# Kernel optimization log

Hardware: AMD Instinct MI355X
Metric: run time of the kernel (lower is better)

Reference implementation:

```python
import jax, jax.numpy as jnp
import numpy as np

M, N, D, P = 16, 4096, 128, 8192
H = N // D


def setup_inputs() -> dict:
    key = jax.random.key(0)
    ks = jax.random.split(key, 6)
    s = 1.0 / np.sqrt(N)
    return {
        "X": jax.random.normal(ks[0], (M, N), dtype=jnp.float32),
        "W_q": jax.random.normal(ks[1], (N, N), dtype=jnp.float32) * s,
        "W_k": jax.random.normal(ks[2], (N, N), dtype=jnp.float32) * s,
        "W_v": jax.random.normal(ks[3], (N, N), dtype=jnp.float32) * s,
        "cache_K": jax.random.normal(ks[4], (H, P, D), dtype=jnp.float32),
        "cache_V": jax.random.normal(ks[5], (H, P, D), dtype=jnp.float32),
    }


def reference(X, W_q, W_k, W_v, cache_K, cache_V):
    m = X.shape[0]
    h, p, d = cache_K.shape
    # QKV projections: [M, N] @ [N, N] -> [M, H, D] -> [H, M, D]
    q = (X @ W_q).reshape(m, h, d).transpose(1, 0, 2)
    k = (X @ W_k).reshape(m, h, d).transpose(1, 0, 2)
    v = (X @ W_v).reshape(m, h, d).transpose(1, 0, 2)
    # KV-cache concat along the sequence axis -> [H, P+M, D]
    k_all = jnp.concatenate([cache_K, k], axis=1)
    v_all = jnp.concatenate([cache_V, v], axis=1)
    # attention (note: original applies NO 1/sqrt(D) scaling)
    scores = jnp.einsum('hmd,hpd->hmp', q, k_all)  # [H, M, P+M]
    weights = jax.nn.softmax(scores, axis=-1)
    out = jnp.einsum('hmp,hpd->hmd', weights, v_all)  # [H, M, D]
    return out.transpose(1, 0, 2).reshape(m, h * d)
```

## Files before the change

### kernel.cpp

```cpp
#include <hip/hip_runtime.h>

#define HN 32
#define MM 16
#define DD 128
#define NN 4096
#define PP 8192
#define TP 64
#define NCH 32
#define CROWS 256

__global__ __launch_bounds__(256) void qkv_kernel(
    const float* __restrict__ X, const float* __restrict__ Wq,
    const float* __restrict__ Wk, const float* __restrict__ Wv,
    float* __restrict__ qkv)
{
    const int bx  = blockIdx.x;
    const int mat = bx >> 8;
    const int r   = bx & 255;
    const int ct  = r >> 5;
    const int rc  = r & 31;
    const int col0 = ct << 9;
    const int i0   = rc << 7;
    const float* W = (mat == 0) ? Wq : (mat == 1) ? Wk : Wv;
    const int t = threadIdx.x;

    const int c0 = col0 + t, c1 = col0 + 256 + t;
    float a0[MM], a1[MM];
#pragma unroll
    for (int m = 0; m < MM; ++m) { a0[m] = 0.f; a1[m] = 0.f; }

    for (int i8 = 0; i8 < 128; i8 += 8) {
        const float* Wr = W + (size_t)(i0 + i8) * NN;
        float w0[8], w1[8];
#pragma unroll
        for (int rr = 0; rr < 8; ++rr) {
            w0[rr] = Wr[(size_t)rr*NN + c0];
            w1[rr] = Wr[(size_t)rr*NN + c1];
        }
        const float* Xr = X + i0 + i8;
#pragma unroll
        for (int m = 0; m < MM; ++m) {
            float4 xa = *reinterpret_cast<const float4*>(Xr + (size_t)m*NN);
            float4 xb = *reinterpret_cast<const float4*>(Xr + (size_t)m*NN + 4);
            a0[m] += xa.x*w0[0] + xa.y*w0[1] + xa.z*w0[2] + xa.w*w0[3]
                   + xb.x*w0[4] + xb.y*w0[5] + xb.z*w0[6] + xb.w*w0[7];
            a1[m] += xa.x*w1[0] + xa.y*w1[1] + xa.z*w1[2] + xa.w*w1[3]
                   + xb.x*w1[4] + xb.y*w1[5] + xb.z*w1[6] + xb.w*w1[7];
        }
    }
    float* base = qkv + (size_t)mat * HN*MM*DD;
    const int h0 = c0 >> 7, d0 = c0 & 127;
    const int h1 = c1 >> 7, d1 = c1 & 127;
#pragma unroll
    for (int m = 0; m < MM; ++m) {
        atomicAdd(&base[(h0*MM + m)*DD + d0], a0[m]);
        atomicAdd(&base[(h1*MM + m)*DD + d1], a1[m]);
    }
}

__global__ __launch_bounds__(256, 2) void attn_partial6(
    const float* __restrict__ cacheK, const float* __restrict__ cacheV,
    const float* __restrict__ qkv, float* __restrict__ pmu,
    float* __restrict__ ps, float* __restrict__ pacc)
{
    __shared__ float Ks[TP][DD + 4];
    __shared__ float Wl[TP][20];

    const int chunk = blockIdx.x;
    const int h     = blockIdx.y;
    const int t     = threadIdx.x;
    const int lane  = t & 63;
    const int wv    = __builtin_amdgcn_readfirstlane((int)(threadIdx.x >> 6));
    const int srow  = t >> 5;
    const int sg    = t & 31;
    const int psi   = lane >> 4;
    const int g     = lane & 15;

    const float* k_ws = qkv + HN*MM*DD;
    const float* v_ws = qkv + 2*HN*MM*DD;
    const int start = chunk * CROWS;
    const float* Kbase = cacheK + ((size_t)h*PP + start)*DD;
    const float* Vbase = cacheV + ((size_t)h*PP + start)*DD;
    const float* qb    = qkv + ((size_t)h*MM + 4*wv)*DD;

    const int ntile = 4 + (chunk == NCH - 1 ? 1 : 0);

    float mu0 = -3.0e38f, mu1 = -3.0e38f, mu2 = -3.0e38f, mu3 = -3.0e38f;
    float ss0 = 0.f, ss1 = 0.f, ss2 = 0.f, ss3 = 0.f;
    float acc[4][8];
#pragma unroll
    for (int q = 0; q < 4; ++q)
#pragma unroll
        for (int k = 0; k < 8; ++k) acc[q][k] = 0.f;

    for (int tt = 0; tt < ntile; ++tt) {
        const bool tail  = (tt == 4);
        const int  valid = tail ? MM : TP;

        const float* srcK = tail ? k_ws + (size_t)h*MM*DD
                                 : Kbase + (size_t)tt*TP*DD;
#pragma unroll
        for (int rr = 0; rr < 8; ++rr) {
            const int row  = srow + 8*rr;
            const int srcr = tail ? min(row, MM - 1) : row;
            float4 kk = *reinterpret_cast<const float4*>(srcK + (size_t)srcr*DD + sg*4);
            *reinterpret_cast<float4*>(&Ks[row][sg*4]) = kk;
        }
        __syncthreads();

        float s0 = 0.f, s1 = 0.f, s2 = 0.f, s3 = 0.f;
#pragma unroll 8
        for (int dq = 0; dq < 32; ++dq) {
            float4 k  = *reinterpret_cast<const float4*>(&Ks[lane][dq*4]);
            const float* qp = qb + dq*4;
            float4 q0 = *reinterpret_cast<const float4*>(qp);
            float4 q1 = *reinterpret_cast<const float4*>(qp + DD);
            float4 q2 = *reinterpret_cast<const float4*>(qp + 2*DD);
            float4 q3 = *reinterpret_cast<const float4*>(qp + 3*DD);
            s0 += k.x*q0.x + k.y*q0.y + k.z*q0.z + k.w*q0.w;
            s1 += k.x*q1.x + k.y*q1.y + k.z*q1.z + k.w*q1.w;
            s2 += k.x*q2.x + k.y*q2.y + k.z*q2.z + k.w*q2.w;
            s3 += k.x*q3.x + k.y*q3.y + k.z*q3.z + k.w*q3.w;
        }
        if (lane >= valid) { s0 = s1 = s2 = s3 = -3.0e38f; }

        float m0 = s0, m1 = s1, m2 = s2, m3 = s3;
#pragma unroll
        for (int off = 1; off < 64; off <<= 1) {
            m0 = fmaxf(m0, __shfl_xor(m0, off));
            m1 = fmaxf(m1, __shfl_xor(m1, off));
            m2 = fmaxf(m2, __shfl_xor(m2, off));
            m3 = fmaxf(m3, __shfl_xor(m3, off));
        }
        const float n0 = fmaxf(mu0, m0), n1 = fmaxf(mu1, m1);
        const float n2 = fmaxf(mu2, m2), n3 = fmaxf(mu3, m3);
        const float r0 = __expf(mu0 - n0), r1 = __expf(mu1 - n1);
        const float r2 = __expf(mu2 - n2), r3 = __expf(mu3 - n3);
        const float w0 = __expf(s0 - n0);
        const float w1 = __expf(s1 - n1);
        const float w2 = __expf(s2 - n2);
        const float w3 = __expf(s3 - n3);
        float t0s = w0, t1s = w1, t2s = w2, t3s = w3;
#pragma unroll
        for (int off = 1; off < 64; off <<= 1) {
            t0s += __shfl_xor(t0s, off);
            t1s += __shfl_xor(t1s, off);
            t2s += __shfl_xor(t2s, off);
            t3s += __shfl_xor(t3s, off);
        }
        ss0 = ss0*r0 + t0s; ss1 = ss1*r1 + t1s;
        ss2 = ss2*r2 + t2s; ss3 = ss3*r3 + t3s;
        mu0 = n0; mu1 = n1; mu2 = n2; mu3 = n3;
        *reinterpret_cast<float4*>(&Wl[lane][4*wv]) = make_float4(w0, w1, w2, w3);

        __syncthreads();

#pragma unroll
        for (int k = 0; k < 8; ++k) {
            acc[0][k] *= r0; acc[1][k] *= r1; acc[2][k] *= r2; acc[3][k] *= r3;
        }
        const float* srcV = tail ? v_ws + (size_t)h*MM*DD
                                 : Vbase + (size_t)tt*TP*DD;
#pragma unroll 4
        for (int i = 0; i < 16; ++i) {
            const int p    = psi + 4*i;
            const int srcr = tail ? min(p, MM - 1) : p;
            const float* vp = srcV + (size_t)srcr*DD + g*8;
            float4 wq = *reinterpret_cast<const float4*>(&Wl[p][4*wv]);
            float4 v0 = *reinterpret_cast<const float4*>(vp);
            float4 v1 = *reinterpret_cast<const float4*>(vp + 4);
            acc[0][0] += wq.x*v0.x; acc[0][1] += wq.x*v0.y; acc[0][2] += wq.x*v0.z; acc[0][3] += wq.x*v0.w;
            acc[0][4] += wq.x*v1.x; acc[0][5] += wq.x*v1.y; acc[0][6] += wq.x*v1.z; acc[0][7] += wq.x*v1.w;
            acc[1][0] += wq.y*v0.x; acc[1][1] += wq.y*v0.y; acc[1][2] += wq.y*v0.z; acc[1][3] += wq.y*v0.w;
            acc[1][4] += wq.y*v1.x; acc[1][5] += wq.y*v1.y; acc[1][6] += wq.y*v1.z; acc[1][7] += wq.y*v1.w;
            acc[2][0] += wq.z*v0.x; acc[2][1] += wq.z*v0.y; acc[2][2] += wq.z*v0.z; acc[2][3] += wq.z*v0.w;
            acc[2][4] += wq.z*v1.x; acc[2][5] += wq.z*v1.y; acc[2][6] += wq.z*v1.z; acc[2][7] += wq.z*v1.w;
            acc[3][0] += wq.w*v0.x; acc[3][1] += wq.w*v0.y; acc[3][2] += wq.w*v0.z; acc[3][3] += wq.w*v0.w;
            acc[3][4] += wq.w*v1.x; acc[3][5] += wq.w*v1.y; acc[3][6] += wq.w*v1.z; acc[3][7] += wq.w*v1.w;
        }
    }

#pragma unroll
    for (int q = 0; q < 4; ++q)
#pragma unroll
        for (int k = 0; k < 8; ++k) {
            float v = acc[q][k];
            v += __shfl_xor(v, 16);
            v += __shfl_xor(v, 32);
            acc[q][k] = v;
        }
    if (lane < 16) {
        float* pa = pacc + ((size_t)(h*NCH + chunk)*MM + 4*wv)*DD;
#pragma unroll
        for (int q = 0; q < 4; ++q) {
            *reinterpret_cast<float4*>(pa + q*DD + g*8) =
                make_float4(acc[q][0], acc[q][1], acc[q][2], acc[q][3]);
            *reinterpret_cast<float4*>(pa + q*DD + g*8 + 4) =
                make_float4(acc[q][4], acc[q][5], acc[q][6], acc[q][7]);
        }
    }
    if (lane == 0) {
        const int o = (h*NCH + chunk)*MM + 4*wv;
        pmu[o + 0] = mu0; pmu[o + 1] = mu1; pmu[o + 2] = mu2; pmu[o + 3] = mu3;
        ps [o + 0] = ss0; ps [o + 1] = ss1; ps [o + 2] = ss2; ps [o + 3] = ss3;
    }
}

__global__ __launch_bounds__(128) void combine_kernel(
    const float* __restrict__ pmu, const float* __restrict__ ps,
    const float* __restrict__ pacc, float* __restrict__ out)
{
    const int b = blockIdx.x;
    const int h = b >> 4, m = b & 15;
    const int d = threadIdx.x;
    float gm = -3.0e38f;
#pragma unroll 8
    for (int c = 0; c < NCH; ++c)
        gm = fmaxf(gm, pmu[(h*NCH + c)*MM + m]);
    float stot = 0.f, a = 0.f;
#pragma unroll 8
    for (int c = 0; c < NCH; ++c) {
        const float f = __expf(pmu[(h*NCH + c)*MM + m] - gm);
        stot += ps[(h*NCH + c)*MM + m] * f;
        a += pacc[((size_t)(h*NCH + c)*MM + m)*DD + d] * f;
    }
    out[m*NN + h*DD + d] = a / stot;
}

extern "C" void kernel_launch(void* const* d_in, const int* in_sizes, int n_in,
                              void* d_out, int out_size, void* d_ws, size_t ws_size,
                              hipStream_t stream) {
    const float* X  = (const float*)d_in[0];
    const float* Wq = (const float*)d_in[1];
    const float* Wk = (const float*)d_in[2];
    const float* Wv = (const float*)d_in[3];
    const float* cK = (const float*)d_in[4];
    const float* cV = (const float*)d_in[5];
    float* out = (float*)d_out;

    float* ws     = (float*)d_ws;
    float* qkv    = ws;
    float* pmu_p  = ws + 3*HN*MM*DD;
    float* ps_p   = pmu_p + HN*NCH*MM;
    float* pacc_p = ps_p + HN*NCH*MM;

    hipMemsetAsync(qkv, 0, (size_t)3*HN*MM*DD*sizeof(float), stream);
    qkv_kernel<<<768, 256, 0, stream>>>(X, Wq, Wk, Wv, qkv);
    attn_partial6<<<dim3(NCH, HN), 256, 0, stream>>>(cK, cV, qkv, pmu_p, ps_p, pacc_p);
    combine_kernel<<<HN*MM, 128, 0, stream>>>(pmu_p, ps_p, pacc_p, out);
}
```

Baseline: 177.6 us.

## Replace QKV atomics with split-K partials plus reduce, halve attention chunks, prefetch K

The QKV projection no longer uses memset plus atomicAdd. Each split-K block writes its partial sums to workspace, and a separate reduce kernel sums them into qkv. The attention kernel now uses 64 chunks of 128 rows instead of 32 of 256, which doubles the grid for more parallelism. It also prefetches the next K tile into registers while the current one is being used. This adds an extra kernel launch and extra workspace traffic for the partials, and raises register pressure in the attention kernel.

```diff
diff --git a/kernel.cpp b/kernel.cpp
--- a/kernel.cpp
+++ b/kernel.cpp
@@ -6,21 +6,22 @@
 #define NN 4096
 #define PP 8192
 #define TP 64
-#define NCH 32
-#define CROWS 256
+#define NCH 64
+#define CROWS 128
 
 __global__ __launch_bounds__(256) void qkv_kernel(
     const float* __restrict__ X, const float* __restrict__ Wq,
     const float* __restrict__ Wk, const float* __restrict__ Wv,
-    float* __restrict__ qkv)
-{
-    const int bx  = blockIdx.x;
-    const int mat = bx >> 8;
-    const int r   = bx & 255;
-    const int ct  = r >> 5;
-    const int rc  = r & 31;
+    float* __restrict__ part, int RC)
+{
+    const int bx   = blockIdx.x;
+    const int mat  = bx / (8 * RC);
+    const int rem  = bx - mat * 8 * RC;
+    const int ct   = rem / RC;
+    const int rcid = rem - ct * RC;
+    const int ROWS = NN / RC;
     const int col0 = ct << 9;
-    const int i0   = rc << 7;
+    const int i0   = rcid * ROWS;
     const float* W = (mat == 0) ? Wq : (mat == 1) ? Wk : Wv;
     const int t = threadIdx.x;
 
@@ -29,36 +30,56 @@
 #pragma unroll
     for (int m = 0; m < MM; ++m) { a0[m] = 0.f; a1[m] = 0.f; }
 
-    for (int i8 = 0; i8 < 128; i8 += 8) {
-        const float* Wr = W + (size_t)(i0 + i8) * NN;
-        float w0[8], w1[8];
-#pragma unroll
-        for (int rr = 0; rr < 8; ++rr) {
+    for (int ib = 0; ib < ROWS; ib += 16) {
+        const float* Wr = W + (size_t)(i0 + ib) * NN;
+        float w0[16], w1[16];
+#pragma unroll
+        for (int rr = 0; rr < 16; ++rr) {
             w0[rr] = Wr[(size_t)rr*NN + c0];
             w1[rr] = Wr[(size_t)rr*NN + c1];
         }
-        const float* Xr = X + i0 + i8;
+        const float* Xr = X + i0 + ib;
 #pragma unroll
         for (int m = 0; m < MM; ++m) {
             float4 xa = *reinterpret_cast<const float4*>(Xr + (size_t)m*NN);
             float4 xb = *reinterpret_cast<const float4*>(Xr + (size_t)m*NN + 4);
+            float4 xc = *reinterpret_cast<const float4*>(Xr + (size_t)m*NN + 8);
+            float4 xd = *reinterpret_cast<const float4*>(Xr + (size_t)m*NN + 12);
             a0[m] += xa.x*w0[0] + xa.y*w0[1] + xa.z*w0[2] + xa.w*w0[3]
-                   + xb.x*w0[4] + xb.y*w0[5] + xb.z*w0[6] + xb.w*w0[7];
+                   + xb.x*w0[4] + xb.y*w0[5] + xb.z*w0[6] + xb.w*w0[7]
+                   + xc.x*w0[8] + xc.y*w0[9] + xc.z*w0[10] + xc.w*w0[11]
+                   + xd.x*w0[12] + xd.y*w0[13] + xd.z*w0[14] + xd.w*w0[15];
             a1[m] += xa.x*w1[0] + xa.y*w1[1] + xa.z*w1[2] + xa.w*w1[3]
-                   + xb.x*w1[4] + xb.y*w1[5] + xb.z*w1[6] + xb.w*w1[7];
-        }
-    }
-    float* base = qkv + (size_t)mat * HN*MM*DD;
-    const int h0 = c0 >> 7, d0 = c0 & 127;
-    const int h1 = c1 >> 7, d1 = c1 & 127;
+                   + xb.x*w1[4] + xb.y*w1[5] + xb.z*w1[6] + xb.w*w1[7]
+                   + xc.x*w1[8] + xc.y*w1[9] + xc.z*w1[10] + xc.w*w1[11]
+                   + xd.x*w1[12] + xd.y*w1[13] + xd.z*w1[14] + xd.w*w1[15];
+        }
+    }
+    float* pb = part + ((size_t)(rcid*3 + mat)*MM)*NN;
 #pragma unroll
     for (int m = 0; m < MM; ++m) {
-        atomicAdd(&base[(h0*MM + m)*DD + d0], a0[m]);
-        atomicAdd(&base[(h1*MM + m)*DD + d1], a1[m]);
-    }
-}
-
-__global__ __launch_bounds__(256, 2) void attn_partial6(
+        pb[(size_t)m*NN + c0] = a0[m];
+        pb[(size_t)m*NN + c1] = a1[m];
+    }
+}
+
+__global__ __launch_bounds__(256) void qkv_reduce(
+    const float* __restrict__ part, float* __restrict__ qkv, int RC)
+{
+    const int o   = blockIdx.x * 256 + threadIdx.x;
+    const int mat = o >> 16;
+    const int r   = o & 65535;
+    const int h   = r >> 11;
+    const int m   = (r >> 7) & 15;
+    const int d   = r & 127;
+    const int col = h * DD + d;
+    const float* p = part + ((size_t)mat*MM + m)*NN + col;
+    float s = 0.f;
+    for (int rc = 0; rc < RC; ++rc) s += p[(size_t)rc * (3*MM*NN)];
+    qkv[o] = s;
+}
+
+__global__ __launch_bounds__(256, 2) void attn_partial7(
     const float* __restrict__ cacheK, const float* __restrict__ cacheV,
     const float* __restrict__ qkv, float* __restrict__ pmu,
     float* __restrict__ ps, float* __restrict__ pacc)
@@ -83,7 +104,7 @@
     const float* Vbase = cacheV + ((size_t)h*PP + start)*DD;
     const float* qb    = qkv + ((size_t)h*MM + 4*wv)*DD;
 
-    const int ntile = 4 + (chunk == NCH - 1 ? 1 : 0);
+    const int ntile = 2 + (chunk == NCH - 1 ? 1 : 0);
 
     float mu0 = -3.0e38f, mu1 = -3.0e38f, mu2 = -3.0e38f, mu3 = -3.0e38f;
     float ss0 = 0.f, ss1 = 0.f, ss2 = 0.f, ss3 = 0.f;
@@ -93,19 +114,33 @@
 #pragma unroll
         for (int k = 0; k < 8; ++k) acc[q][k] = 0.f;
 
+    float4 stK[8];
+    auto issueK = [&](int tt2) {
+        if (tt2 < 2) {
+            const float* B = Kbase + (size_t)(tt2*TP)*DD;
+#pragma unroll
+            for (int rr = 0; rr < 8; ++rr)
+                stK[rr] = *reinterpret_cast<const float4*>(B + (size_t)(srow + 8*rr)*DD + sg*4);
+        } else {
+#pragma unroll
+            for (int rr = 0; rr < 8; ++rr) {
+                const int srcr = min(srow + 8*rr, MM - 1);
+                stK[rr] = *reinterpret_cast<const float4*>(k_ws + ((size_t)h*MM + srcr)*DD + sg*4);
+            }
+        }
+    };
+
+    issueK(0);
+
     for (int tt = 0; tt < ntile; ++tt) {
-        const bool tail  = (tt == 4);
+        const bool tail  = (tt == 2);
         const int  valid = tail ? MM : TP;
 
-        const float* srcK = tail ? k_ws + (size_t)h*MM*DD
-                                 : Kbase + (size_t)tt*TP*DD;
-#pragma unroll
-        for (int rr = 0; rr < 8; ++rr) {
-            const int row  = srow + 8*rr;
-            const int srcr = tail ? min(row, MM - 1) : row;
-            float4 kk = *reinterpret_cast<const float4*>(srcK + (size_t)srcr*DD + sg*4);
-            *reinterpret_cast<float4*>(&Ks[row][sg*4]) = kk;
-        }
+#pragma unroll
+        for (int rr = 0; rr < 8; ++rr)
+            *reinterpret_cast<float4*>(&Ks[srow + 8*rr][sg*4]) = stK[rr];
+        if (tt + 1 < ntile) issueK(tt + 1);
+
         __syncthreads();
 
         float s0 = 0.f, s1 = 0.f, s2 = 0.f, s3 = 0.f;
@@ -238,14 +273,20 @@
     const float* cV = (const float*)d_in[5];
     float* out = (float*)d_out;
 
+    const size_t QKVF = (size_t)3*HN*MM*DD;
+    const size_t favail = ws_size / sizeof(float);
+    int RC = 32;
+    if (favail < QKVF + 32*QKVF) RC = 16;
+
     float* ws     = (float*)d_ws;
     float* qkv    = ws;
-    float* pmu_p  = ws + 3*HN*MM*DD;
+    float* part   = ws + QKVF;
+    float* pmu_p  = ws + QKVF;
     float* ps_p   = pmu_p + HN*NCH*MM;
     float* pacc_p = ps_p + HN*NCH*MM;
 
-    hipMemsetAsync(qkv, 0, (size_t)3*HN*MM*DD*sizeof(float), stream);
-    qkv_kernel<<<768, 256, 0, stream>>>(X, Wq, Wk, Wv, qkv);
-    attn_partial6<<<dim3(NCH, HN), 256, 0, stream>>>(cK, cV, qkv, pmu_p, ps_p, pacc_p);
+    qkv_kernel<<<3*8*RC, 256, 0, stream>>>(X, Wq, Wk, Wv, part, RC);
+    qkv_reduce<<<768, 256, 0, stream>>>(part, qkv, RC);
+    attn_partial7<<<dim3(NCH, HN), 256, 0, stream>>>(cK, cV, qkv, pmu_p, ps_p, pacc_p);
     combine_kernel<<<HN*MM, 128, 0, stream>>>(pmu_p, ps_p, pacc_p, out);
 }
```

Result: slower. 271.0 us (+52.6%).
